# Optimization experiments

Measured on AMD Instinct MI355X. Metric: run time of the kernel, lower is better.

## Reference

```python
import jax, jax.numpy as jnp
import numpy as np

B, T, D = 2, 1024, 2048
H, K, DK = 4, 8, 64
E = 16384
NK = 128  # sqrt(num_experts)


def setup_inputs() -> dict:
    key = jax.random.key(0)
    k1, k2, k3, k4, k5 = jax.random.split(key, 5)
    x = jax.random.normal(k1, (B, T, D), dtype=jnp.float32)
    Wq = jax.random.normal(k2, (D, 2 * H * DK), dtype=jnp.float32) * 0.02
    keys = jax.random.normal(k3, (H, NK, 2, DK), dtype=jnp.float32) * 0.02
    e_down = jax.random.normal(k4, (E, D), dtype=jnp.float32) * 0.01
    e_up = jax.random.normal(k5, (E, D), dtype=jnp.float32) * 0.01
    return {"x": x, "Wq": Wq, "keys": keys, "e_down": e_down, "e_up": e_up}


def reference(x, Wq, keys, e_down, e_up):
    b, t, d = x.shape
    # queries: [B,T,h,2,dk] (torch Linear: x @ W^T; Wq stored as [in,out])
    q = (x @ Wq).reshape(b, t, H, 2, DK)
    q1, q2 = q[..., 0, :], q[..., 1, :]
    sim1 = jnp.einsum('bthd,hkd->bthk', q1, keys[:, :, 0, :])  # [B,T,h,NK]
    sim2 = jnp.einsum('bthd,hkd->bthk', q2, keys[:, :, 1, :])
    s1, i1 = jax.lax.top_k(sim1, K)  # [B,T,h,K]
    s2, i2 = jax.lax.top_k(sim2, K)
    # k x k cross product of the two sub-key topks
    all_scores = (s1[..., :, None] + s2[..., None, :]).reshape(b, t, H, K * K)
    all_indices = (i1[..., :, None] * NK + i2[..., None, :]).reshape(b, t, H, K * K)
    final_scores, pk_idx = jax.lax.top_k(all_scores, K)  # [B,T,h,K]
    final_indices = jnp.take_along_axis(all_indices, pk_idx, axis=-1)
    w_down = e_down[final_indices]  # [B,T,h,K,D] gather
    w_up = e_up[final_indices]      # [B,T,h,K,D] gather
    hidden = jnp.einsum('btd,bthkd->bthk', x, w_down)
    hidden = jax.nn.silu(hidden)
    hidden = hidden * jax.nn.relu(final_scores)  # non_competing=True
    out = jnp.einsum('bthk,bthkd->btd', hidden, w_up)
    return out
```

## Files before the change

### kernel.cpp

```cpp
#include <hip/hip_runtime.h>
#include <math.h>

#define Bsz 2
#define Tsz 1024
#define Dsz 2048
#define Hn 4
#define Kn 8
#define DKn 64
#define En 16384
#define NKn 128
#define NTOK (Bsz * Tsz)
#define QCOLS (2 * Hn * DKn)
#define KSPLIT 4
#define KCHUNK (Dsz / KSPLIT)

#define GM 64
#define GN 64
#define GK 16

__global__ __launch_bounds__(256) void gemm_q_kernel(
    const float* __restrict__ A,
    const float* __restrict__ B,
    float* __restrict__ P)
{
    const int K = Dsz, N = QCOLS;
    __shared__ float As[GK][GM + 4];
    __shared__ float Bs[GK][GN + 4];

    const int tid = threadIdx.x;
    const int row0 = blockIdx.x * GM;
    const int col0 = blockIdx.y * GN;
    const int k0 = blockIdx.z * KCHUNK;
    const int tx = tid & 15;
    const int ty = tid >> 4;

    const int am = tid >> 2;
    const int ak = (tid & 3) << 2;
    const int bk = tid >> 4;
    const int bn = (tid & 15) << 2;

    float acc[4][4] = {};

    for (int kt = k0; kt < k0 + KCHUNK; kt += GK) {
        float4 av = *(const float4*)(A + (size_t)(row0 + am) * K + kt + ak);
        float4 bv = *(const float4*)(B + (size_t)(kt + bk) * N + col0 + bn);
        As[ak + 0][am] = av.x;
        As[ak + 1][am] = av.y;
        As[ak + 2][am] = av.z;
        As[ak + 3][am] = av.w;
        *(float4*)&Bs[bk][bn] = bv;
        __syncthreads();
#pragma unroll
        for (int k = 0; k < GK; k++) {
            float4 a = *(const float4*)&As[k][ty << 2];
            float4 b = *(const float4*)&Bs[k][tx << 2];
            acc[0][0] = fmaf(a.x, b.x, acc[0][0]);
            acc[0][1] = fmaf(a.x, b.y, acc[0][1]);
            acc[0][2] = fmaf(a.x, b.z, acc[0][2]);
            acc[0][3] = fmaf(a.x, b.w, acc[0][3]);
            acc[1][0] = fmaf(a.y, b.x, acc[1][0]);
            acc[1][1] = fmaf(a.y, b.y, acc[1][1]);
            acc[1][2] = fmaf(a.y, b.z, acc[1][2]);
            acc[1][3] = fmaf(a.y, b.w, acc[1][3]);
            acc[2][0] = fmaf(a.z, b.x, acc[2][0]);
            acc[2][1] = fmaf(a.z, b.y, acc[2][1]);
            acc[2][2] = fmaf(a.z, b.z, acc[2][2]);
            acc[2][3] = fmaf(a.z, b.w, acc[2][3]);
            acc[3][0] = fmaf(a.w, b.x, acc[3][0]);
            acc[3][1] = fmaf(a.w, b.y, acc[3][1]);
            acc[3][2] = fmaf(a.w, b.z, acc[3][2]);
            acc[3][3] = fmaf(a.w, b.w, acc[3][3]);
        }
        __syncthreads();
    }

    float* Pz = P + (size_t)blockIdx.z * NTOK * QCOLS;
#pragma unroll
    for (int i = 0; i < 4; i++) {
        float4 cv = make_float4(acc[i][0], acc[i][1], acc[i][2], acc[i][3]);
        *(float4*)(Pz + (size_t)(row0 + (ty << 2) + i) * N + col0 + (tx << 2)) = cv;
    }
}

__device__ inline void argmax64d(double& v, int& i) {
#pragma unroll
    for (int off = 1; off < 64; off <<= 1) {
        double ov = __shfl_xor(v, off);
        int oi = __shfl_xor(i, off);
        if (ov > v || (ov == v && oi < i)) { v = ov; i = oi; }
    }
}

__global__ __launch_bounds__(64) void select_kernel(
    const float* __restrict__ P,
    const float* __restrict__ keys,
    int* __restrict__ fidx,
    float* __restrict__ fscore)
{
    const int bth = blockIdx.x;
    const int token = bth >> 2;
    const int h = bth & 3;
    const int lane = threadIdx.x;

    __shared__ __align__(16) float q1s[64];
    __shared__ __align__(16) float q2s[64];
    {
        const float* qp = P + (size_t)token * QCOLS + h * 128;
        double q1d = 0., q2d = 0.;
#pragma unroll
        for (int s = 0; s < KSPLIT; s++) {
            q1d += (double)qp[(size_t)s * NTOK * QCOLS + lane];
            q2d += (double)qp[(size_t)s * NTOK * QCOLS + 64 + lane];
        }
        q1s[lane] = (float)q1d;
        q2s[lane] = (float)q2d;
    }
    __syncthreads();

    const float* kb = keys + (size_t)h * (NKn * 2 * DKn);
    const float4* ka0 = (const float4*)(kb + (size_t)(lane * 2 + 0) * DKn);
    const float4* ka1 = (const float4*)(kb + (size_t)((lane + 64) * 2 + 0) * DKn);
    const float4* kc0 = (const float4*)(kb + (size_t)(lane * 2 + 1) * DKn);
    const float4* kc1 = (const float4*)(kb + (size_t)((lane + 64) * 2 + 1) * DKn);
    const float4* q1v = (const float4*)q1s;
    const float4* q2v = (const float4*)q2s;

    double a0 = 0., a1 = 0., b0 = 0., b1 = 0.;
#pragma unroll
    for (int d = 0; d < DKn / 4; d++) {
        float4 q1 = q1v[d], q2 = q2v[d];
        float4 x0 = ka0[d], x1 = ka1[d], y0 = kc0[d], y1 = kc1[d];
        a0 = fma((double)q1.x, (double)x0.x, a0);
        a0 = fma((double)q1.y, (double)x0.y, a0);
        a0 = fma((double)q1.z, (double)x0.z, a0);
        a0 = fma((double)q1.w, (double)x0.w, a0);
        a1 = fma((double)q1.x, (double)x1.x, a1);
        a1 = fma((double)q1.y, (double)x1.y, a1);
        a1 = fma((double)q1.z, (double)x1.z, a1);
        a1 = fma((double)q1.w, (double)x1.w, a1);
        b0 = fma((double)q2.x, (double)y0.x, b0);
        b0 = fma((double)q2.y, (double)y0.y, b0);
        b0 = fma((double)q2.z, (double)y0.z, b0);
        b0 = fma((double)q2.w, (double)y0.w, b0);
        b1 = fma((double)q2.x, (double)y1.x, b1);
        b1 = fma((double)q2.y, (double)y1.y, b1);
        b1 = fma((double)q2.z, (double)y1.z, b1);
        b1 = fma((double)q2.w, (double)y1.w, b1);
    }

    double myS1 = 0., myS2 = 0.;
    int myI1 = 0, myI2 = 0;
    {
        double c0 = a0, c1 = a1;
#pragma unroll
        for (int r = 0; r < Kn; r++) {
            double v; int i;
            if (c1 > c0) { v = c1; i = lane + 64; } else { v = c0; i = lane; }
            argmax64d(v, i);
            if ((lane >> 3) == r) { myS1 = v; myI1 = i; }
            if (i == lane) c0 = -INFINITY;
            else if (i == lane + 64) c1 = -INFINITY;
        }
    }
    {
        double c0 = b0, c1 = b1;
#pragma unroll
        for (int r = 0; r < Kn; r++) {
            double v; int i;
            if (c1 > c0) { v = c1; i = lane + 64; } else { v = c0; i = lane; }
            argmax64d(v, i);
            if ((lane & 7) == r) { myS2 = v; myI2 = i; }
            if (i == lane) c0 = -INFINITY;
            else if (i == lane + 64) c1 = -INFINITY;
        }
    }

    double c = myS1 + myS2;
    const int pidx = myI1 * NKn + myI2;
    double outS = 0.;
    int outI = 0;
#pragma unroll
    for (int r = 0; r < Kn; r++) {
        double v = c; int i = lane;
        argmax64d(v, i);
        int widx = __shfl(pidx, i);
        if (lane == r) { outS = v; outI = widx; }
        if (i == lane) c = -INFINITY;
    }

    if (lane < Kn) {
        fscore[(size_t)bth * Kn + lane] = (float)outS;
        fidx[(size_t)bth * Kn + lane] = outI;
    }
}

__device__ inline float dot4(float4 a, float4 b) {
    return a.x * b.x + a.y * b.y + a.z * b.z + a.w * b.w;
}

__global__ __launch_bounds__(256) void expert_kernel(
    const float* __restrict__ x,
    const float* __restrict__ e_down,
    const float* __restrict__ e_up,
    const int* __restrict__ fidx,
    const float* __restrict__ fscore,
    float* __restrict__ out)
{
    const int token = blockIdx.x;
    const int tid = threadIdx.x;
    const int wid = tid >> 6;
    const int lane = tid & 63;

    __shared__ float xs[Dsz];
    __shared__ float red[Dsz];

    {
        const float4* xr = (const float4*)(x + (size_t)token * Dsz);
        float4* xv = (float4*)xs;
        xv[tid] = xr[tid];
        xv[tid + 256] = xr[tid + 256];
    }
    __syncthreads();

    const float4* xv = (const float4*)xs;

    float4 acc[8];
#pragma unroll
    for (int j = 0; j < 8; j++) acc[j] = make_float4(0.f, 0.f, 0.f, 0.f);

    const int* fi = fidx + (size_t)token * (Hn * Kn);
    const float* fs = fscore + (size_t)token * (Hn * Kn);

#pragma unroll 1
    for (int i = 0; i < 8; i++) {
        const int e = wid * 8 + i;
        const int idx = fi[e];
        const float sc = fs[e];
        const float4* wd = (const float4*)(e_down + (size_t)idx * Dsz);
        const float4* wu = (const float4*)(e_up + (size_t)idx * Dsz);

        float4 dv[8], uv[8];
#pragma unroll
        for (int j = 0; j < 8; j++) dv[j] = wd[lane + j * 64];
#pragma unroll
        for (int j = 0; j < 8; j++) uv[j] = wu[lane + j * 64];

        float p = 0.f;
#pragma unroll
        for (int j = 0; j < 8; j++) p += dot4(xv[lane + j * 64], dv[j]);
#pragma unroll
        for (int off = 1; off < 64; off <<= 1) p += __shfl_xor(p, off);

        const float act = (p / (1.f + expf(-p))) * fmaxf(sc, 0.f);
#pragma unroll
        for (int j = 0; j < 8; j++) {
            acc[j].x = fmaf(act, uv[j].x, acc[j].x);
            acc[j].y = fmaf(act, uv[j].y, acc[j].y);
            acc[j].z = fmaf(act, uv[j].z, acc[j].z);
            acc[j].w = fmaf(act, uv[j].w, acc[j].w);
        }
    }

    __syncthreads();
#pragma unroll 1
    for (int w = 0; w < 4; w++) {
        if (wid == w) {
            if (w == 0) {
#pragma unroll
                for (int j = 0; j < 8; j++)
                    *(float4*)&red[(lane + j * 64) * 4] = acc[j];
            } else {
#pragma unroll
                for (int j = 0; j < 8; j++) {
                    float4 r = *(const float4*)&red[(lane + j * 64) * 4];
                    r.x += acc[j].x; r.y += acc[j].y;
                    r.z += acc[j].z; r.w += acc[j].w;
                    *(float4*)&red[(lane + j * 64) * 4] = r;
                }
            }
        }
        __syncthreads();
    }

    float4* o = (float4*)(out + (size_t)token * Dsz);
    const float4* rv = (const float4*)red;
    o[tid] = rv[tid];
    o[tid + 256] = rv[tid + 256];
}

extern "C" void kernel_launch(void* const* d_in, const int* in_sizes, int n_in,
                              void* d_out, int out_size, void* d_ws, size_t ws_size,
                              hipStream_t stream) {
    const float* x      = (const float*)d_in[0];
    const float* Wq     = (const float*)d_in[1];
    const float* keys   = (const float*)d_in[2];
    const float* e_down = (const float*)d_in[3];
    const float* e_up   = (const float*)d_in[4];
    float* out = (float*)d_out;

    float* P = (float*)d_ws;
    int* fidx = (int*)((char*)d_ws + (size_t)(16 << 20));
    float* fscore = (float*)((char*)d_ws + (size_t)(16 << 20) + (256 << 10));

    dim3 g1(NTOK / GM, QCOLS / GN, KSPLIT);
    gemm_q_kernel<<<g1, 256, 0, stream>>>(x, Wq, P);

    select_kernel<<<NTOK * Hn, 64, 0, stream>>>(P, keys, fidx, fscore);

    expert_kernel<<<NTOK, 256, 0, stream>>>(x, e_down, e_up, fidx, fscore, out);
}
```

Baseline: 577.3 us.

## Transpose sub-keys for coalesced select loads and prefetch GEMM tiles

Adds a small kernel that transposes the keys tensor into a [h][s][d][n] layout. This lets the select kernel read keys coalesced across lanes, where before each lane strode through its own key row. Separately, the Q-projection GEMM now loads the next global tile into registers before computing on the current shared-memory tile, to overlap load latency with FMAs. The cost is an extra kernel launch and more workspace use.

Result: faster. 493.0 us (-14.6%).

```diff
diff --git a/kernel.cpp b/kernel.cpp
--- a/kernel.cpp
+++ b/kernel.cpp
@@ -14,6 +14,18 @@
 #define KSPLIT 4
 #define KCHUNK (Dsz / KSPLIT)
 
+__global__ __launch_bounds__(256) void transpose_keys_kernel(
+    const float* __restrict__ keys, float* __restrict__ keysT)
+{
+    const int idx = blockIdx.x * 256 + threadIdx.x;
+    const int h = idx >> 14;
+    const int rem = idx & 16383;
+    const int n = rem >> 7;
+    const int s = (rem >> 6) & 1;
+    const int d = rem & 63;
+    keysT[(((size_t)h * 2 + s) * DKn + d) * NKn + n] = keys[idx];
+}
+
 #define GM 64
 #define GN 64
 #define GK 16
@@ -41,15 +53,22 @@
 
     float acc[4][4] = {};
 
+    float4 av = *(const float4*)(A + (size_t)(row0 + am) * K + k0 + ak);
+    float4 bv = *(const float4*)(B + (size_t)(k0 + bk) * N + col0 + bn);
+
     for (int kt = k0; kt < k0 + KCHUNK; kt += GK) {
-        float4 av = *(const float4*)(A + (size_t)(row0 + am) * K + kt + ak);
-        float4 bv = *(const float4*)(B + (size_t)(kt + bk) * N + col0 + bn);
         As[ak + 0][am] = av.x;
         As[ak + 1][am] = av.y;
         As[ak + 2][am] = av.z;
         As[ak + 3][am] = av.w;
         *(float4*)&Bs[bk][bn] = bv;
         __syncthreads();
+
+        if (kt + GK < k0 + KCHUNK) {
+            av = *(const float4*)(A + (size_t)(row0 + am) * K + (kt + GK) + ak);
+            bv = *(const float4*)(B + (size_t)(kt + GK + bk) * N + col0 + bn);
+        }
+
 #pragma unroll
         for (int k = 0; k < GK; k++) {
             float4 a = *(const float4*)&As[k][ty << 2];
@@ -93,7 +112,7 @@
 
 __global__ __launch_bounds__(64) void select_kernel(
     const float* __restrict__ P,
-    const float* __restrict__ keys,
+    const float* __restrict__ keysT,
     int* __restrict__ fidx,
     float* __restrict__ fscore)
 {
@@ -117,35 +136,21 @@
     }
     __syncthreads();
 
-    const float* kb = keys + (size_t)h * (NKn * 2 * DKn);
-    const float4* ka0 = (const float4*)(kb + (size_t)(lane * 2 + 0) * DKn);
-    const float4* ka1 = (const float4*)(kb + (size_t)((lane + 64) * 2 + 0) * DKn);
-    const float4* kc0 = (const float4*)(kb + (size_t)(lane * 2 + 1) * DKn);
-    const float4* kc1 = (const float4*)(kb + (size_t)((lane + 64) * 2 + 1) * DKn);
-    const float4* q1v = (const float4*)q1s;
-    const float4* q2v = (const float4*)q2s;
+    const float* kT = keysT + (size_t)h * (2 * DKn * NKn);
 
     double a0 = 0., a1 = 0., b0 = 0., b1 = 0.;
-#pragma unroll
-    for (int d = 0; d < DKn / 4; d++) {
-        float4 q1 = q1v[d], q2 = q2v[d];
-        float4 x0 = ka0[d], x1 = ka1[d], y0 = kc0[d], y1 = kc1[d];
-        a0 = fma((double)q1.x, (double)x0.x, a0);
-        a0 = fma((double)q1.y, (double)x0.y, a0);
-        a0 = fma((double)q1.z, (double)x0.z, a0);
-        a0 = fma((double)q1.w, (double)x0.w, a0);
-        a1 = fma((double)q1.x, (double)x1.x, a1);
-        a1 = fma((double)q1.y, (double)x1.y, a1);
-        a1 = fma((double)q1.z, (double)x1.z, a1);
-        a1 = fma((double)q1.w, (double)x1.w, a1);
-        b0 = fma((double)q2.x, (double)y0.x, b0);
-        b0 = fma((double)q2.y, (double)y0.y, b0);
-        b0 = fma((double)q2.z, (double)y0.z, b0);
-        b0 = fma((double)q2.w, (double)y0.w, b0);
-        b1 = fma((double)q2.x, (double)y1.x, b1);
-        b1 = fma((double)q2.y, (double)y1.y, b1);
-        b1 = fma((double)q2.z, (double)y1.z, b1);
-        b1 = fma((double)q2.w, (double)y1.w, b1);
+#pragma unroll 8
+    for (int d = 0; d < DKn; d++) {
+        const double q1 = (double)q1s[d];
+        const double q2 = (double)q2s[d];
+        const float k0a = kT[d * NKn + lane];
+        const float k1a = kT[d * NKn + lane + 64];
+        const float k0b = kT[(DKn + d) * NKn + lane];
+        const float k1b = kT[(DKn + d) * NKn + lane + 64];
+        a0 = fma(q1, (double)k0a, a0);
+        a1 = fma(q1, (double)k1a, a1);
+        b0 = fma(q2, (double)k0b, b0);
+        b1 = fma(q2, (double)k1b, b1);
     }
 
     double myS1 = 0., myS2 = 0.;
@@ -301,11 +306,14 @@
     float* P = (float*)d_ws;
     int* fidx = (int*)((char*)d_ws + (size_t)(16 << 20));
     float* fscore = (float*)((char*)d_ws + (size_t)(16 << 20) + (256 << 10));
+    float* keysT = (float*)((char*)d_ws + (size_t)(16 << 20) + (512 << 10));
+
+    transpose_keys_kernel<<<256, 256, 0, stream>>>(keys, keysT);
 
     dim3 g1(NTOK / GM, QCOLS / GN, KSPLIT);
     gemm_q_kernel<<<g1, 256, 0, stream>>>(x, Wq, P);
 
-    select_kernel<<<NTOK * Hn, 64, 0, stream>>>(P, keys, fidx, fscore);
+    select_kernel<<<NTOK * Hn, 64, 0, stream>>>(P, keysT, fidx, fscore);
 
     expert_kernel<<<NTOK, 256, 0, stream>>>(x, e_down, e_up, fidx, fscore, out);
 }
```
